# Kernel optimization log

Measured on AMD Instinct MI355X. Metric: run time of the kernel, lower is better.

## Reference

```python
import jax, jax.numpy as jnp
import numpy as np

N_SRC = 50000
N_DST = 50000
E = 800000
IN_DIM = 128
OUT_DIM = 64
HEADS = 4
NEG_SLOPE = 0.2  # PyG GATConv default negative_slope
EPS = 1e-16      # PyG softmax denominator epsilon


def setup_inputs() -> dict:
    key = jax.random.key(0)
    ks = jax.random.split(key, 8)
    x_src = jax.random.normal(ks[0], (N_SRC, IN_DIM), dtype=jnp.float32)
    x_dst = jax.random.normal(ks[1], (N_DST, IN_DIM), dtype=jnp.float32)
    src = jax.random.randint(ks[2], (E,), 0, N_SRC, dtype=jnp.int32)
    dst = jax.random.randint(ks[3], (E,), 0, N_DST, dtype=jnp.int32)
    edge_index = jnp.stack([src, dst], axis=0)
    W_src = jax.random.normal(ks[4], (IN_DIM, HEADS * OUT_DIM), dtype=jnp.float32) / np.sqrt(IN_DIM)
    W_dst = jax.random.normal(ks[5], (IN_DIM, HEADS * OUT_DIM), dtype=jnp.float32) / np.sqrt(IN_DIM)
    att_src = jax.random.normal(ks[6], (HEADS, OUT_DIM), dtype=jnp.float32) / np.sqrt(OUT_DIM)
    att_dst = jax.random.normal(ks[7], (HEADS, OUT_DIM), dtype=jnp.float32) / np.sqrt(OUT_DIM)
    bias = jnp.zeros((OUT_DIM,), dtype=jnp.float32)
    return {"x_src": x_src, "x_dst": x_dst, "edge_index": edge_index,
            "W_src": W_src, "W_dst": W_dst, "att_src": att_src,
            "att_dst": att_dst, "bias": bias}


def reference(x_src, x_dst, edge_index, W_src, W_dst, att_src, att_dst, bias):
    # Linear projections -> [N, H, C]
    hs = (x_src @ W_src).reshape(N_SRC, HEADS, OUT_DIM)
    hd = (x_dst @ W_dst).reshape(N_DST, HEADS, OUT_DIM)
    # Per-node attention logits -> [N, H]
    a_s = jnp.einsum('nhc,hc->nh', hs, att_src)
    a_d = jnp.einsum('nhc,hc->nh', hd, att_dst)

    src, dst = edge_index[0], edge_index[1]
    # Per-edge logits [E, H]
    alpha = jax.nn.leaky_relu(a_s[src] + a_d[dst], negative_slope=NEG_SLOPE)
    # Segment softmax over edges sharing the same dst node
    amax = jax.ops.segment_max(alpha, dst, num_segments=N_DST)
    alpha = jnp.exp(alpha - amax[dst])
    denom = jax.ops.segment_sum(alpha, dst, num_segments=N_DST)
    alpha = alpha / (denom[dst] + EPS)
    # (dropout=0 / eval mode: no attention dropout)
    # Message + scatter-add aggregation: out[i] = sum_e alpha_e * hs[src_e]
    msg = hs[src] * alpha[:, :, None]                 # [E, H, C]
    out = jax.ops.segment_sum(msg, dst, num_segments=N_DST)  # [N_dst, H, C]
    # concat=False -> mean over heads, then bias
    return out.mean(axis=1) + bias
```

## Files before the change

kernel.cpp:

```cpp
#include <hip/hip_runtime.h>
#include <hip/hip_bf16.h>

#define N_SRC 50000
#define N_DST 50000
#define NEDGE 800000
#define IND   128
#define HEADS 4
#define CDIM  64
#define HC    256
#define NB_SCAN 49

typedef _Float16 half8 __attribute__((ext_vector_type(8)));
typedef float    f32x4 __attribute__((ext_vector_type(4)));

__global__ void prep_kernel(const float* __restrict__ Wdst,
                            const float* __restrict__ att_d,
                            float* __restrict__ WdA,
                            const float* __restrict__ Wsrc,
                            _Float16* __restrict__ WhT, int* __restrict__ deg) {
    int b = blockIdx.x, tid = threadIdx.x;
    if (b < 196) {
        int i = b * 256 + tid;
        if (i < N_DST) deg[i] = 0;
    } else if (b < 198) {
        int id = (b - 196) * 256 + tid;
        int k = id >> 2, h = id & 3;
        float acc = 0.f;
        for (int c = 0; c < CDIM; ++c)
            acc += Wdst[k * HC + h * CDIM + c] * att_d[h * CDIM + c];
        WdA[id] = acc;
    } else {
        int idx = (b - 198) * 256 + tid;
        int n = idx >> 7, k = idx & 127;
        WhT[idx] = (_Float16)Wsrc[k * HC + n];
    }
}

__global__ __launch_bounds__(256) void node_alpha_kernel(
        const float* __restrict__ x_dst, const float* __restrict__ WdA,
        float* __restrict__ a_d) {
    int n    = (blockIdx.x * 256 + threadIdx.x) >> 6;
    int lane = threadIdx.x & 63;
    const float* xp = x_dst + (size_t)n * IND;
    const float4* wa = (const float4*)WdA;
    float x0 = xp[lane], x1 = xp[lane + 64];
    float4 wa0 = wa[lane], wa1 = wa[lane + 64];
    float p0 = x0 * wa0.x + x1 * wa1.x;
    float p1 = x0 * wa0.y + x1 * wa1.y;
    float p2 = x0 * wa0.z + x1 * wa1.z;
    float p3 = x0 * wa0.w + x1 * wa1.w;
    for (int off = 32; off >= 1; off >>= 1) {
        p0 += __shfl_xor(p0, off, 64);
        p1 += __shfl_xor(p1, off, 64);
        p2 += __shfl_xor(p2, off, 64);
        p3 += __shfl_xor(p3, off, 64);
    }
    if (lane == 0) {
        a_d[n * 4 + 0] = p0; a_d[n * 4 + 1] = p1;
        a_d[n * 4 + 2] = p2; a_d[n * 4 + 3] = p3;
    }
}

__global__ __launch_bounds__(256) void gemm_mfma_kernel(
        const float* __restrict__ x, const _Float16* __restrict__ WhT,
        const float* __restrict__ att_s,
        __hip_bfloat16* __restrict__ hsTb, float* __restrict__ a_s) {
    int tid = threadIdx.x;
    int w = tid >> 6, lane = tid & 63;
    int ll = lane & 15, q = lane >> 4;
    int rbase = blockIdx.x * 64 + w * 16;

    int arow = rbase + ll;
    if (arow >= N_SRC) arow = N_SRC - 1;
    const float* xr = x + (size_t)arow * IND + q * 8;
    half8 afrag[4];
    #pragma unroll
    for (int kf = 0; kf < 4; ++kf) {
        float4 u0 = *(const float4*)(xr + kf * 32);
        float4 u1 = *(const float4*)(xr + kf * 32 + 4);
        half8 a;
        a[0] = (_Float16)u0.x; a[1] = (_Float16)u0.y;
        a[2] = (_Float16)u0.z; a[3] = (_Float16)u0.w;
        a[4] = (_Float16)u1.x; a[5] = (_Float16)u1.y;
        a[6] = (_Float16)u1.z; a[7] = (_Float16)u1.w;
        afrag[kf] = a;
    }

    f32x4 acc[16];
    #pragma unroll
    for (int t = 0; t < 16; ++t) acc[t] = (f32x4){0.f, 0.f, 0.f, 0.f};

    #pragma unroll
    for (int t = 0; t < 16; ++t) {
        const _Float16* bp = WhT + (size_t)(t * 16 + ll) * IND + q * 8;
        half8 b0 = *(const half8*)(bp + 0);
        half8 b1 = *(const half8*)(bp + 32);
        half8 b2 = *(const half8*)(bp + 64);
        half8 b3 = *(const half8*)(bp + 96);
        f32x4 c = acc[t];
        c = __builtin_amdgcn_mfma_f32_16x16x32_f16(afrag[0], b0, c, 0, 0, 0);
        c = __builtin_amdgcn_mfma_f32_16x16x32_f16(afrag[1], b1, c, 0, 0, 0);
        c = __builtin_amdgcn_mfma_f32_16x16x32_f16(afrag[2], b2, c, 0, 0, 0);
        c = __builtin_amdgcn_mfma_f32_16x16x32_f16(afrag[3], b3, c, 0, 0, 0);
        acc[t] = c;
    }

    #pragma unroll
    for (int tg = 0; tg < 4; ++tg) {
        #pragma unroll
        for (int r = 0; r < 4; ++r) {
            int n = rbase + q * 4 + r;
            if (n < N_SRC) {
                __hip_bfloat16 h0 = __float2bfloat16(acc[tg     ][r]);
                __hip_bfloat16 h1 = __float2bfloat16(acc[tg + 4 ][r]);
                __hip_bfloat16 h2 = __float2bfloat16(acc[tg + 8 ][r]);
                __hip_bfloat16 h3 = __float2bfloat16(acc[tg + 12][r]);
                unsigned int lo = *(unsigned short*)&h0 | ((unsigned int)*(unsigned short*)&h1 << 16);
                unsigned int hi = *(unsigned short*)&h2 | ((unsigned int)*(unsigned short*)&h3 << 16);
                uint2 v = {lo, hi};
                *(uint2*)((unsigned short*)hsTb + (size_t)n * HC + (tg * 16 + ll) * 4) = v;
            }
        }
    }

    float attv[16];
    #pragma unroll
    for (int t = 0; t < 16; ++t) attv[t] = att_s[t * 16 + ll];
    #pragma unroll
    for (int r = 0; r < 4; ++r) {
        float4 p;
        p.x = acc[0][r]*attv[0]  + acc[1][r]*attv[1]  + acc[2][r]*attv[2]  + acc[3][r]*attv[3];
        p.y = acc[4][r]*attv[4]  + acc[5][r]*attv[5]  + acc[6][r]*attv[6]  + acc[7][r]*attv[7];
        p.z = acc[8][r]*attv[8]  + acc[9][r]*attv[9]  + acc[10][r]*attv[10]+ acc[11][r]*attv[11];
        p.w = acc[12][r]*attv[12]+ acc[13][r]*attv[13]+ acc[14][r]*attv[14]+ acc[15][r]*attv[15];
        #pragma unroll
        for (int off = 1; off < 16; off <<= 1) {
            p.x += __shfl_xor(p.x, off, 64);
            p.y += __shfl_xor(p.y, off, 64);
            p.z += __shfl_xor(p.z, off, 64);
            p.w += __shfl_xor(p.w, off, 64);
        }
        int n = rbase + q * 4 + r;
        if (ll == 0 && n < N_SRC) *(float4*)(a_s + (size_t)n * 4) = p;
    }
}

__global__ void hist_kernel(const int* __restrict__ dst, int* __restrict__ deg,
                            int* __restrict__ rank) {
    int e = blockIdx.x * 256 + threadIdx.x;
    if (e < NEDGE) rank[e] = atomicAdd(&deg[dst[e]], 1);
}

__global__ __launch_bounds__(256) void scan_part_kernel(const int* __restrict__ deg,
                                                        int* __restrict__ partial) {
    __shared__ int wsum[4];
    int tid = threadIdx.x, lane = tid & 63, wid = tid >> 6;
    int i0 = blockIdx.x * 1024 + tid * 4;
    int s = 0;
    #pragma unroll
    for (int j = 0; j < 4; ++j) if (i0 + j < N_DST) s += deg[i0 + j];
    for (int off = 32; off >= 1; off >>= 1) s += __shfl_xor(s, off, 64);
    if (lane == 0) wsum[wid] = s;
    __syncthreads();
    if (tid == 0) partial[blockIdx.x] = wsum[0] + wsum[1] + wsum[2] + wsum[3];
}

__global__ __launch_bounds__(256) void scan_write_kernel(const int* __restrict__ deg,
                                                         const int* __restrict__ partial,
                                                         int* __restrict__ row_ptr) {
    __shared__ int wsum[4];
    __shared__ int block_off;
    int tid = threadIdx.x, lane = tid & 63, wid = tid >> 6;
    if (tid < 64) {
        int v = (lane < NB_SCAN) ? partial[lane] : 0;
        int xx = v;
        for (int off = 1; off < 64; off <<= 1) {
            int u = __shfl_up(xx, off, 64);
            if (lane >= off) xx += u;
        }
        if (lane == blockIdx.x) block_off = xx - v;
    }
    int i0 = blockIdx.x * 1024 + tid * 4;
    int v0 = (i0 + 0 < N_DST) ? deg[i0 + 0] : 0;
    int v1 = (i0 + 1 < N_DST) ? deg[i0 + 1] : 0;
    int v2 = (i0 + 2 < N_DST) ? deg[i0 + 2] : 0;
    int v3 = (i0 + 3 < N_DST) ? deg[i0 + 3] : 0;
    int t1 = v0, t2 = t1 + v1, t3 = t2 + v2, t4 = t3 + v3;
    int x = t4;
    for (int off = 1; off < 64; off <<= 1) {
        int u = __shfl_up(x, off, 64);
        if (lane >= off) x += u;
    }
    int wave_excl = x - t4;
    if (lane == 63) wsum[wid] = x;
    __syncthreads();
    int woff = 0;
    for (int k = 0; k < wid; ++k) woff += wsum[k];
    int tb = block_off + woff + wave_excl;
    if (i0 + 0 < N_DST) row_ptr[i0 + 0] = tb;
    if (i0 + 1 < N_DST) row_ptr[i0 + 1] = tb + t1;
    if (i0 + 2 < N_DST) row_ptr[i0 + 2] = tb + t2;
    if (i0 + 3 < N_DST) row_ptr[i0 + 3] = tb + t3;
    if (blockIdx.x == 0 && tid == 0) row_ptr[N_DST] = NEDGE;
}

__global__ void scatter_kernel(const int* __restrict__ src, const int* __restrict__ dst,
                               const int* __restrict__ row_ptr,
                               const int* __restrict__ rank, int* __restrict__ col) {
    int e = blockIdx.x * 256 + threadIdx.x;
    if (e >= NEDGE) return;
    int d = dst[e];
    col[row_ptr[d] + rank[e]] = src[e];
}

#define ACC8(W, H)                                   \
    a0 += (W).x * __uint_as_float((H).x << 16);      \
    a1 += (W).y * __uint_as_float((H).x & 0xffff0000u); \
    a2 += (W).z * __uint_as_float((H).y << 16);      \
    a3 += (W).w * __uint_as_float((H).y & 0xffff0000u);

__global__ __launch_bounds__(256) void aggregate_kernel(
        const int* __restrict__ row_ptr, const int* __restrict__ col,
        const float4* __restrict__ as4, const float4* __restrict__ ad4,
        const __hip_bfloat16* __restrict__ hsTb,
        const float* __restrict__ bias, float* __restrict__ out) {
    __shared__ int    s_off[4][64];
    __shared__ float4 s_w[4][64];
    int tid = threadIdx.x;
    int wv = tid >> 6, lane = tid & 63;
    int i = (blockIdx.x * 256 + tid) >> 6;
    if (i >= N_DST) return;
    int beg = row_ptr[i], end = row_ptr[i + 1];
    float bv = bias[lane];
    if (beg == end) { out[i * CDIM + lane] = bv; return; }
    float4 ad = ad4[i];

    const unsigned short* hb = (const unsigned short*)hsTb + (lane << 2);
    float s0 = 0.f, s1 = 0.f, s2 = 0.f, s3 = 0.f;
    float a0 = 0.f, a1 = 0.f, a2 = 0.f, a3 = 0.f;

    for (int cb = beg; cb < end; cb += 64) {
        int e = cb + lane;
        bool valid = e < end;
        int sn = valid ? col[e] : 0;
        float4 av = as4[sn];
        float lx = av.x + ad.x; lx = lx > 0.f ? lx : 0.2f * lx;
        float ly = av.y + ad.y; ly = ly > 0.f ? ly : 0.2f * ly;
        float lz = av.z + ad.z; lz = lz > 0.f ? lz : 0.2f * lz;
        float lw = av.w + ad.w; lw = lw > 0.f ? lw : 0.2f * lw;
        float4 wq;
        wq.x = valid ? __expf(lx) : 0.f;
        wq.y = valid ? __expf(ly) : 0.f;
        wq.z = valid ? __expf(lz) : 0.f;
        wq.w = valid ? __expf(lw) : 0.f;
        s0 += wq.x; s1 += wq.y; s2 += wq.z; s3 += wq.w;
        s_off[wv][lane] = sn * HC;
        s_w[wv][lane]   = wq;
        __asm__ volatile("s_waitcnt lgkmcnt(0)" ::: "memory");

        int cnt = end - cb; if (cnt > 64) cnt = 64;
        int j = 0;
        for (; j + 4 <= cnt; j += 4) {
            int o0 = s_off[wv][j];     float4 q0 = s_w[wv][j];
            int o1 = s_off[wv][j + 1]; float4 q1 = s_w[wv][j + 1];
            int o2 = s_off[wv][j + 2]; float4 q2 = s_w[wv][j + 2];
            int o3 = s_off[wv][j + 3]; float4 q3 = s_w[wv][j + 3];
            uint2 h0 = *(const uint2*)(hb + o0);
            uint2 h1 = *(const uint2*)(hb + o1);
            uint2 h2 = *(const uint2*)(hb + o2);
            uint2 h3 = *(const uint2*)(hb + o3);
            ACC8(q0, h0) ACC8(q1, h1) ACC8(q2, h2) ACC8(q3, h3)
        }
        for (; j < cnt; ++j) {
            int o0 = s_off[wv][j]; float4 q0 = s_w[wv][j];
            uint2 h0 = *(const uint2*)(hb + o0);
            ACC8(q0, h0)
        }
    }
    for (int off = 32; off >= 1; off >>= 1) {
        s0 += __shfl_xor(s0, off, 64);
        s1 += __shfl_xor(s1, off, 64);
        s2 += __shfl_xor(s2, off, 64);
        s3 += __shfl_xor(s3, off, 64);
    }
    out[i * CDIM + lane] = 0.25f * (a0 / (s0 + 1e-16f) + a1 / (s1 + 1e-16f)
                                  + a2 / (s2 + 1e-16f) + a3 / (s3 + 1e-16f)) + bv;
}

extern "C" void kernel_launch(void* const* d_in, const int* in_sizes, int n_in,
                              void* d_out, int out_size, void* d_ws, size_t ws_size,
                              hipStream_t stream) {
    const float* x_src   = (const float*)d_in[0];
    const float* x_dst   = (const float*)d_in[1];
    const int*   ei      = (const int*)d_in[2];
    const float* W_src   = (const float*)d_in[3];
    const float* W_dst   = (const float*)d_in[4];
    const float* att_src = (const float*)d_in[5];
    const float* att_dst = (const float*)d_in[6];
    const float* bias    = (const float*)d_in[7];
    float* out = (float*)d_out;

    char* ws = (char*)d_ws;
    __hip_bfloat16* hsTb = (__hip_bfloat16*)ws; ws += (size_t)N_SRC * HC * 2;
    int*    col     = (int*)ws;    ws += (size_t)NEDGE * 4;
    int*    rank    = (int*)ws;    ws += (size_t)NEDGE * 4;
    float*  a_s     = (float*)ws;  ws += (size_t)N_SRC * 4 * 4;
    float*  a_d     = (float*)ws;  ws += (size_t)N_DST * 4 * 4;
    float*  WdA     = (float*)ws;  ws += 2048;
    _Float16* WhT   = (_Float16*)ws; ws += IND * HC * 2;
    int*    row_ptr = (int*)ws;    ws += 50004 * 4;
    int*    deg     = (int*)ws;    ws += N_DST * 4;
    int*    partial = (int*)ws;    ws += 64 * 4;

    prep_kernel<<<326, 256, 0, stream>>>(W_dst, att_dst, WdA, W_src, WhT, deg);
    gemm_mfma_kernel<<<(N_SRC + 63) / 64, 256, 0, stream>>>(x_src, WhT, att_src, hsTb, a_s);
    node_alpha_kernel<<<N_DST / 4, 256, 0, stream>>>(x_dst, WdA, a_d);
    hist_kernel<<<NEDGE / 256, 256, 0, stream>>>(ei + NEDGE, deg, rank);
    scan_part_kernel<<<NB_SCAN, 256, 0, stream>>>(deg, partial);
    scan_write_kernel<<<NB_SCAN, 256, 0, stream>>>(deg, partial, row_ptr);
    scatter_kernel<<<NEDGE / 256, 256, 0, stream>>>(ei, ei + NEDGE, row_ptr, rank, col);
    aggregate_kernel<<<(N_DST + 3) / 4, 256, 0, stream>>>(row_ptr, col,
                                                          (const float4*)a_s, (const float4*)a_d,
                                                          hsTb, bias, out);
}
```

Baseline: 262.0 us.

## Store projected features in fp16 and aggregate with fdot2 using pre-normalized weights

The projected source features are now stored as fp16 instead of bf16. The aggregate kernel becomes two-pass: it first computes the softmax denominators, then builds normalized fp16 weights packed with offsets in shared memory and accumulates with fdot2 into a single accumulator. This replaces four bf16 unpack-and-FMA chains per edge and drops the final divides. The node-alpha and histogram kernels are merged into one launch. The trade-offs are a second pass over col and a_s with recomputed exponentials, and fp16 precision and range risk in the features and weights.

```diff
diff --git a/kernel.cpp b/kernel.cpp
--- a/kernel.cpp
+++ b/kernel.cpp
@@ -9,9 +9,21 @@
 #define CDIM  64
 #define HC    256
 #define NB_SCAN 49
-
-typedef _Float16 half8 __attribute__((ext_vector_type(8)));
-typedef float    f32x4 __attribute__((ext_vector_type(4)));
+#define NB_ALPHA 12500
+#define NB_HIST  3125
+
+typedef _Float16 half8  __attribute__((ext_vector_type(8)));
+typedef _Float16 half2t __attribute__((ext_vector_type(2)));
+typedef float    f32x4  __attribute__((ext_vector_type(4)));
+
+static __device__ __forceinline__ unsigned int pack2h(float a, float b) {
+    union { half2t h; unsigned int u; } v;
+    v.h[0] = (_Float16)a; v.h[1] = (_Float16)b;
+    return v.u;
+}
+static __device__ __forceinline__ half2t bits2h(unsigned int u) {
+    union { unsigned int u; half2t h; } v; v.u = u; return v.h;
+}
 
 __global__ void prep_kernel(const float* __restrict__ Wdst,
                             const float* __restrict__ att_d,
@@ -36,35 +48,10 @@
     }
 }
 
-__global__ __launch_bounds__(256) void node_alpha_kernel(
-        const float* __restrict__ x_dst, const float* __restrict__ WdA,
-        float* __restrict__ a_d) {
-    int n    = (blockIdx.x * 256 + threadIdx.x) >> 6;
-    int lane = threadIdx.x & 63;
-    const float* xp = x_dst + (size_t)n * IND;
-    const float4* wa = (const float4*)WdA;
-    float x0 = xp[lane], x1 = xp[lane + 64];
-    float4 wa0 = wa[lane], wa1 = wa[lane + 64];
-    float p0 = x0 * wa0.x + x1 * wa1.x;
-    float p1 = x0 * wa0.y + x1 * wa1.y;
-    float p2 = x0 * wa0.z + x1 * wa1.z;
-    float p3 = x0 * wa0.w + x1 * wa1.w;
-    for (int off = 32; off >= 1; off >>= 1) {
-        p0 += __shfl_xor(p0, off, 64);
-        p1 += __shfl_xor(p1, off, 64);
-        p2 += __shfl_xor(p2, off, 64);
-        p3 += __shfl_xor(p3, off, 64);
-    }
-    if (lane == 0) {
-        a_d[n * 4 + 0] = p0; a_d[n * 4 + 1] = p1;
-        a_d[n * 4 + 2] = p2; a_d[n * 4 + 3] = p3;
-    }
-}
-
 __global__ __launch_bounds__(256) void gemm_mfma_kernel(
         const float* __restrict__ x, const _Float16* __restrict__ WhT,
         const float* __restrict__ att_s,
-        __hip_bfloat16* __restrict__ hsTb, float* __restrict__ a_s) {
+        unsigned short* __restrict__ hsTh, float* __restrict__ a_s) {
     int tid = threadIdx.x;
     int w = tid >> 6, lane = tid & 63;
     int ll = lane & 15, q = lane >> 4;
@@ -111,14 +98,10 @@
         for (int r = 0; r < 4; ++r) {
             int n = rbase + q * 4 + r;
             if (n < N_SRC) {
-                __hip_bfloat16 h0 = __float2bfloat16(acc[tg     ][r]);
-                __hip_bfloat16 h1 = __float2bfloat16(acc[tg + 4 ][r]);
-                __hip_bfloat16 h2 = __float2bfloat16(acc[tg + 8 ][r]);
-                __hip_bfloat16 h3 = __float2bfloat16(acc[tg + 12][r]);
-                unsigned int lo = *(unsigned short*)&h0 | ((unsigned int)*(unsigned short*)&h1 << 16);
-                unsigned int hi = *(unsigned short*)&h2 | ((unsigned int)*(unsigned short*)&h3 << 16);
-                uint2 v = {lo, hi};
-                *(uint2*)((unsigned short*)hsTb + (size_t)n * HC + (tg * 16 + ll) * 4) = v;
+                uint2 v;
+                v.x = pack2h(acc[tg     ][r], acc[tg + 4 ][r]);
+                v.y = pack2h(acc[tg + 8 ][r], acc[tg + 12][r]);
+                *(uint2*)(hsTh + (size_t)n * HC + (tg * 16 + ll) * 4) = v;
             }
         }
     }
@@ -145,10 +128,36 @@
     }
 }
 
-__global__ void hist_kernel(const int* __restrict__ dst, int* __restrict__ deg,
-                            int* __restrict__ rank) {
-    int e = blockIdx.x * 256 + threadIdx.x;
-    if (e < NEDGE) rank[e] = atomicAdd(&deg[dst[e]], 1);
+__global__ __launch_bounds__(256) void mid_kernel(
+        const float* __restrict__ x_dst, const float* __restrict__ WdA,
+        float* __restrict__ a_d,
+        const int* __restrict__ dst, int* __restrict__ deg, int* __restrict__ rank) {
+    int b = blockIdx.x, tid = threadIdx.x;
+    if (b < NB_ALPHA) {
+        int n    = (b * 256 + tid) >> 6;
+        int lane = tid & 63;
+        const float* xp = x_dst + (size_t)n * IND;
+        const float4* wa = (const float4*)WdA;
+        float x0 = xp[lane], x1 = xp[lane + 64];
+        float4 wa0 = wa[lane], wa1 = wa[lane + 64];
+        float p0 = x0 * wa0.x + x1 * wa1.x;
+        float p1 = x0 * wa0.y + x1 * wa1.y;
+        float p2 = x0 * wa0.z + x1 * wa1.z;
+        float p3 = x0 * wa0.w + x1 * wa1.w;
+        for (int off = 32; off >= 1; off >>= 1) {
+            p0 += __shfl_xor(p0, off, 64);
+            p1 += __shfl_xor(p1, off, 64);
+            p2 += __shfl_xor(p2, off, 64);
+            p3 += __shfl_xor(p3, off, 64);
+        }
+        if (lane == 0) {
+            a_d[n * 4 + 0] = p0; a_d[n * 4 + 1] = p1;
+            a_d[n * 4 + 2] = p2; a_d[n * 4 + 3] = p3;
+        }
+    } else {
+        int e = (b - NB_ALPHA) * 256 + tid;
+        if (e < NEDGE) rank[e] = atomicAdd(&deg[dst[e]], 1);
+    }
 }
 
 __global__ __launch_bounds__(256) void scan_part_kernel(const int* __restrict__ deg,
@@ -213,19 +222,12 @@
     col[row_ptr[d] + rank[e]] = src[e];
 }
 
-#define ACC8(W, H)                                   \
-    a0 += (W).x * __uint_as_float((H).x << 16);      \
-    a1 += (W).y * __uint_as_float((H).x & 0xffff0000u); \
-    a2 += (W).z * __uint_as_float((H).y << 16);      \
-    a3 += (W).w * __uint_as_float((H).y & 0xffff0000u);
-
 __global__ __launch_bounds__(256) void aggregate_kernel(
         const int* __restrict__ row_ptr, const int* __restrict__ col,
         const float4* __restrict__ as4, const float4* __restrict__ ad4,
-        const __hip_bfloat16* __restrict__ hsTb,
+        const unsigned short* __restrict__ hsTh,
         const float* __restrict__ bias, float* __restrict__ out) {
-    __shared__ int    s_off[4][64];
-    __shared__ float4 s_w[4][64];
+    __shared__ uint4 s_pk[4][64];
     int tid = threadIdx.x;
     int wv = tid >> 6, lane = tid & 63;
     int i = (blockIdx.x * 256 + tid) >> 6;
@@ -235,10 +237,7 @@
     if (beg == end) { out[i * CDIM + lane] = bv; return; }
     float4 ad = ad4[i];
 
-    const unsigned short* hb = (const unsigned short*)hsTb + (lane << 2);
     float s0 = 0.f, s1 = 0.f, s2 = 0.f, s3 = 0.f;
-    float a0 = 0.f, a1 = 0.f, a2 = 0.f, a3 = 0.f;
-
     for (int cb = beg; cb < end; cb += 64) {
         int e = cb + lane;
         bool valid = e < end;
@@ -248,34 +247,10 @@
         float ly = av.y + ad.y; ly = ly > 0.f ? ly : 0.2f * ly;
         float lz = av.z + ad.z; lz = lz > 0.f ? lz : 0.2f * lz;
         float lw = av.w + ad.w; lw = lw > 0.f ? lw : 0.2f * lw;
-        float4 wq;
-        wq.x = valid ? __expf(lx) : 0.f;
-        wq.y = valid ? __expf(ly) : 0.f;
-        wq.z = valid ? __expf(lz) : 0.f;
-        wq.w = valid ? __expf(lw) : 0.f;
-        s0 += wq.x; s1 += wq.y; s2 += wq.z; s3 += wq.w;
-        s_off[wv][lane] = sn * HC;
-        s_w[wv][lane]   = wq;
-        __asm__ volatile("s_waitcnt lgkmcnt(0)" ::: "memory");
-
-        int cnt = end - cb; if (cnt > 64) cnt = 64;
-        int j = 0;
-        for (; j + 4 <= cnt; j += 4) {
-            int o0 = s_off[wv][j];     float4 q0 = s_w[wv][j];
-            int o1 = s_off[wv][j + 1]; float4 q1 = s_w[wv][j + 1];
-            int o2 = s_off[wv][j + 2]; float4 q2 = s_w[wv][j + 2];
-            int o3 = s_off[wv][j + 3]; float4 q3 = s_w[wv][j + 3];
-            uint2 h0 = *(const uint2*)(hb + o0);
-            uint2 h1 = *(const uint2*)(hb + o1);
-            uint2 h2 = *(const uint2*)(hb + o2);
-            uint2 h3 = *(const uint2*)(hb + o3);
-            ACC8(q0, h0) ACC8(q1, h1) ACC8(q2, h2) ACC8(q3, h3)
-        }
-        for (; j < cnt; ++j) {
-            int o0 = s_off[wv][j]; float4 q0 = s_w[wv][j];
-            uint2 h0 = *(const uint2*)(hb + o0);
-            ACC8(q0, h0)
-        }
+        s0 += valid ? __expf(lx) : 0.f;
+        s1 += valid ? __expf(ly) : 0.f;
+        s2 += valid ? __expf(lz) : 0.f;
+        s3 += valid ? __expf(lw) : 0.f;
     }
     for (int off = 32; off >= 1; off >>= 1) {
         s0 += __shfl_xor(s0, off, 64);
@@ -283,8 +258,62 @@
         s2 += __shfl_xor(s2, off, 64);
         s3 += __shfl_xor(s3, off, 64);
     }
-    out[i * CDIM + lane] = 0.25f * (a0 / (s0 + 1e-16f) + a1 / (s1 + 1e-16f)
-                                  + a2 / (s2 + 1e-16f) + a3 / (s3 + 1e-16f)) + bv;
+    float i0 = 0.25f / (s0 + 1e-16f);
+    float i1 = 0.25f / (s1 + 1e-16f);
+    float i2 = 0.25f / (s2 + 1e-16f);
+    float i3 = 0.25f / (s3 + 1e-16f);
+
+    const unsigned short* hb = hsTh + (lane << 2);
+    float acc = 0.f;
+    for (int cb = beg; cb < end; cb += 64) {
+        int e = cb + lane;
+        bool valid = e < end;
+        int sn = valid ? col[e] : 0;
+        float4 av = as4[sn];
+        float lx = av.x + ad.x; lx = lx > 0.f ? lx : 0.2f * lx;
+        float ly = av.y + ad.y; ly = ly > 0.f ? ly : 0.2f * ly;
+        float lz = av.z + ad.z; lz = lz > 0.f ? lz : 0.2f * lz;
+        float lw = av.w + ad.w; lw = lw > 0.f ? lw : 0.2f * lw;
+        float w0 = valid ? __expf(lx) * i0 : 0.f;
+        float w1 = valid ? __expf(ly) * i1 : 0.f;
+        float w2 = valid ? __expf(lz) * i2 : 0.f;
+        float w3 = valid ? __expf(lw) * i3 : 0.f;
+        uint4 pk;
+        pk.x = (unsigned int)(sn * HC);
+        pk.y = pack2h(w0, w1);
+        pk.z = pack2h(w2, w3);
+        pk.w = 0;
+        s_pk[wv][lane] = pk;
+        __asm__ volatile("s_waitcnt lgkmcnt(0)" ::: "memory");
+
+        int cnt = end - cb; if (cnt > 64) cnt = 64;
+        int j = 0;
+        for (; j + 4 <= cnt; j += 4) {
+            uint4 p0 = s_pk[wv][j];
+            uint4 p1 = s_pk[wv][j + 1];
+            uint4 p2 = s_pk[wv][j + 2];
+            uint4 p3 = s_pk[wv][j + 3];
+            uint2 h0 = *(const uint2*)(hb + p0.x);
+            uint2 h1 = *(const uint2*)(hb + p1.x);
+            uint2 h2 = *(const uint2*)(hb + p2.x);
+            uint2 h3 = *(const uint2*)(hb + p3.x);
+            acc = __builtin_amdgcn_fdot2(bits2h(h0.x), bits2h(p0.y), acc, false);
+            acc = __builtin_amdgcn_fdot2(bits2h(h0.y), bits2h(p0.z), acc, false);
+            acc = __builtin_amdgcn_fdot2(bits2h(h1.x), bits2h(p1.y), acc, false);
+            acc = __builtin_amdgcn_fdot2(bits2h(h1.y), bits2h(p1.z), acc, false);
+            acc = __builtin_amdgcn_fdot2(bits2h(h2.x), bits2h(p2.y), acc, false);
+            acc = __builtin_amdgcn_fdot2(bits2h(h2.y), bits2h(p2.z), acc, false);
+            acc = __builtin_amdgcn_fdot2(bits2h(h3.x), bits2h(p3.y), acc, false);
+            acc = __builtin_amdgcn_fdot2(bits2h(h3.y), bits2h(p3.z), acc, false);
+        }
+        for (; j < cnt; ++j) {
+            uint4 p0 = s_pk[wv][j];
+            uint2 h0 = *(const uint2*)(hb + p0.x);
+            acc = __builtin_amdgcn_fdot2(bits2h(h0.x), bits2h(p0.y), acc, false);
+            acc = __builtin_amdgcn_fdot2(bits2h(h0.y), bits2h(p0.z), acc, false);
+        }
+    }
+    out[i * CDIM + lane] = acc + bv;
 }
 
 extern "C" void kernel_launch(void* const* d_in, const int* in_sizes, int n_in,
@@ -301,7 +330,7 @@
     float* out = (float*)d_out;
 
     char* ws = (char*)d_ws;
-    __hip_bfloat16* hsTb = (__hip_bfloat16*)ws; ws += (size_t)N_SRC * HC * 2;
+    unsigned short* hsTh = (unsigned short*)ws; ws += (size_t)N_SRC * HC * 2;
     int*    col     = (int*)ws;    ws += (size_t)NEDGE * 4;
     int*    rank    = (int*)ws;    ws += (size_t)NEDGE * 4;
     float*  a_s     = (float*)ws;  ws += (size_t)N_SRC * 4 * 4;
@@ -313,13 +342,12 @@
     int*    partial = (int*)ws;    ws += 64 * 4;
 
     prep_kernel<<<326, 256, 0, stream>>>(W_dst, att_dst, WdA, W_src, WhT, deg);
-    gemm_mfma_kernel<<<(N_SRC + 63) / 64, 256, 0, stream>>>(x_src, WhT, att_src, hsTb, a_s);
-    node_alpha_kernel<<<N_DST / 4, 256, 0, stream>>>(x_dst, WdA, a_d);
-    hist_kernel<<<NEDGE / 256, 256, 0, stream>>>(ei + NEDGE, deg, rank);
+    gemm_mfma_kernel<<<(N_SRC + 63) / 64, 256, 0, stream>>>(x_src, WhT, att_src, hsTh, a_s);
+    mid_kernel<<<NB_ALPHA + NB_HIST, 256, 0, stream>>>(x_dst, WdA, a_d, ei + NEDGE, deg, rank);
     scan_part_kernel<<<NB_SCAN, 256, 0, stream>>>(deg, partial);
     scan_write_kernel<<<NB_SCAN, 256, 0, stream>>>(deg, partial, row_ptr);
     scatter_kernel<<<NEDGE / 256, 256, 0, stream>>>(ei, ei + NEDGE, row_ptr, rank, col);
     aggregate_kernel<<<(N_DST + 3) / 4, 256, 0, stream>>>(row_ptr, col,
                                                           (const float4*)a_s, (const float4*)a_d,
-                                                          hsTb, bias, out);
-}
+                                                          hsTh, bias, out);
+}
```

After: 260.6 us. No clear change (-0.5%).
